# Kernel tuning notes

Hardware: AMD Instinct MI355X
Metric: run time of the kernel (lower is better)

Reference implementation:

```python
import jax, jax.numpy as jnp
import numpy as np

N_NODES = 100000
N_EDGES = 1600000
IN_FEATS = 256
N_HEADS = 4
OUT_FEATS = 32
NEG_SLOPE = 0.2


def setup_inputs() -> dict:
    key = jax.random.key(0)
    k0, k1, k2, k3, k4, k5 = jax.random.split(key, 6)
    feat = jax.random.normal(k0, (N_NODES, IN_FEATS), dtype=jnp.float32)
    src = jax.random.randint(k1, (N_EDGES,), 0, N_NODES, dtype=jnp.int32)
    dst = jax.random.randint(k2, (N_EDGES,), 0, N_NODES, dtype=jnp.int32)
    # fc.weight: [num_heads*out_feats, in_feats] (torch Linear layout)
    W = jax.random.normal(k3, (N_HEADS * OUT_FEATS, IN_FEATS), dtype=jnp.float32) * 0.05
    attn_l = jax.random.normal(k4, (1, N_HEADS, OUT_FEATS), dtype=jnp.float32) * 0.1
    attn_r = jax.random.normal(k5, (1, N_HEADS, OUT_FEATS), dtype=jnp.float32) * 0.1
    return {"feat": feat, "src": src, "dst": dst, "W": W, "attn_l": attn_l, "attn_r": attn_r}


def reference(feat, src, dst, W, attn_l, attn_r):
    N = feat.shape[0]
    H, D = attn_l.shape[1], attn_l.shape[2]
    # fc projection -> [N, H, D]
    feat_src = (feat @ W.T).reshape(N, H, D)
    el = jnp.sum(feat_src * attn_l, axis=-1)  # [N, H]
    er = jnp.sum(feat_src * attn_r, axis=-1)  # [N, H]
    # per-edge scores: u_add_v then LeakyReLU  -> [E, H]
    e = jax.nn.leaky_relu(el[src] + er[dst], negative_slope=NEG_SLOPE)
    # edge_softmax: segmented softmax over edges grouped by destination node
    emax = jax.ops.segment_max(e, dst, num_segments=N)  # [N, H]
    emax = jnp.where(jnp.isfinite(emax), emax, jnp.zeros_like(emax))
    ee = jnp.exp(e - emax[dst])  # [E, H]
    denom = jax.ops.segment_sum(ee, dst, num_segments=N)  # [N, H]
    a = ee / denom[dst]  # [E, H]
    # u_mul_e + sum aggregation -> [N, H, D]
    m = feat_src[src] * a[:, :, None]  # [E, H, D]
    rst = jax.ops.segment_sum(m, dst, num_segments=N)
    return rst
```

## Files before the change

kernel.cpp:

```cpp
#include <hip/hip_runtime.h>
#include <hip/hip_bf16.h>
#include <math.h>

#define NN 100000
#define NE 1600000
#define INF_ 256
#define NH 4
#define DH 32
#define NHD 128
#define NEG_SLOPE 0.2f

#define NBC 391
#define STRIDEC 4608
#define EPBC 8192
#define NBLK_BIN 196
#define GEMM_BLKS 782
#define FMAX 1408
#define SMEM_BYTES 32768

typedef __attribute__((ext_vector_type(8))) short bf16x8;
typedef __attribute__((ext_vector_type(4))) float f32x4;

__device__ __forceinline__ unsigned short f2bf(float f) {
    __hip_bfloat16 b = __float2bfloat16(f);
    return *reinterpret_cast<unsigned short*>(&b);
}

__global__ __launch_bounds__(256) void k_prep0(const float* __restrict__ W,
                                               unsigned short* __restrict__ Wimg,
                                               int* __restrict__ gcurP) {
    int t = threadIdx.x;
    int b = blockIdx.x;
    if (b == 16) {
        for (int i = t; i < NBC; i += 256) gcurP[i * 16] = 0;
        return;
    }
    int i = b * 256 + t;
    int kt = i >> 9;
    int r = (i >> 2) & 127;
    int g = i & 3;
    int slot = g ^ (r & 7);
    const float* s = &W[(size_t)r * INF_ + kt * 32 + g * 8];
    unsigned short tmp[8];
#pragma unroll
    for (int j = 0; j < 8; j++) tmp[j] = f2bf(s[j]);
    *(bf16x8*)&Wimg[(size_t)kt * 8192 + r * 64 + slot * 8] = *(const bf16x8*)tmp;
}

__global__ __launch_bounds__(256) void k_gemmbin(const float* __restrict__ feat,
                                                 const unsigned short* __restrict__ Wimg,
                                                 const int* __restrict__ src,
                                                 const int* __restrict__ dst,
                                                 const float* __restrict__ al,
                                                 const float* __restrict__ ar,
                                                 unsigned short* __restrict__ fsb,
                                                 float* __restrict__ el,
                                                 float* __restrict__ er,
                                                 int* __restrict__ gcurP,
                                                 unsigned* __restrict__ packed) {
    __shared__ __align__(16) char smem[SMEM_BYTES];
    const int t = threadIdx.x;

    if (blockIdx.x >= GEMM_BLKS) {
        int hb = blockIdx.x - GEMM_BLKS;
        int* lc = (int*)smem;
        int* wb = ((int*)smem) + NBC;
        for (int i = t; i < NBC; i += 256) lc[i] = 0;
        __syncthreads();
        int base = hb * EPBC;
#pragma unroll 4
        for (int j = 0; j < 32; j++) {
            int e = base + j * 256 + t;
            if (e < NE) atomicAdd(&lc[dst[e] >> 8], 1);
        }
        __syncthreads();
        for (int i = t; i < NBC; i += 256) {
            int c = lc[i];
            wb[i] = c ? i * STRIDEC + atomicAdd(&gcurP[i * 16], c) : 0;
            lc[i] = 0;
        }
        __syncthreads();
#pragma unroll 4
        for (int j = 0; j < 32; j++) {
            int e = base + j * 256 + t;
            if (e < NE) {
                int d = dst[e];
                int bk = d >> 8;
                int pos = wb[bk] + atomicAdd(&lc[bk], 1);
                if (pos < (bk + 1) * STRIDEC)
                    packed[pos] = ((unsigned)src[e] << 8) | (unsigned)(d & 255);
            }
        }
        return;
    }

    short* sA = (short*)smem;
    short* sB = (short*)(smem + 16384);
    const int brow = blockIdx.x * 128;
    const int wid = t >> 6, lane = t & 63;
    const int wr = wid >> 1, wc = wid & 1;
    const int lg = lane >> 4;
    const int lr = lane & 15;

    f32x4 acc[4][4];
#pragma unroll
    for (int m = 0; m < 4; m++)
#pragma unroll
        for (int n = 0; n < 4; n++) acc[m][n] = (f32x4){0.f, 0.f, 0.f, 0.f};

    const int srow = t >> 1;
    const int cb = (t & 1) * 16;
    const int g0 = cb >> 3;
    const int p0 = (g0 ^ (srow & 7));
    const int p1 = ((g0 + 1) ^ (srow & 7));
    const int grow = brow + srow;
    const bool arow_ok = (grow < NN);
    const char* bimg = (const char*)Wimg;

    float fv[16];
    uint4 wv0, wv1, wv2, wv3;
    if (arow_ok) {
        const float4* pa = (const float4*)&feat[(size_t)grow * INF_ + cb];
        *(float4*)&fv[0] = pa[0];
        *(float4*)&fv[4] = pa[1];
        *(float4*)&fv[8] = pa[2];
        *(float4*)&fv[12] = pa[3];
    } else {
#pragma unroll
        for (int j = 0; j < 16; j++) fv[j] = 0.f;
    }
    wv0 = *(const uint4*)(bimg + t * 16);
    wv1 = *(const uint4*)(bimg + 4096 + t * 16);
    wv2 = *(const uint4*)(bimg + 8192 + t * 16);
    wv3 = *(const uint4*)(bimg + 12288 + t * 16);

    for (int kt = 0; kt < 8; kt++) {
        {
            short sv[16];
#pragma unroll
            for (int j = 0; j < 16; j++) sv[j] = (short)f2bf(fv[j]);
            *(bf16x8*)&sA[srow * 64 + p0 * 8] = *(const bf16x8*)&sv[0];
            *(bf16x8*)&sA[srow * 64 + p1 * 8] = *(const bf16x8*)&sv[8];
            char* bd = (char*)sB;
            *(uint4*)(bd + t * 16) = wv0;
            *(uint4*)(bd + 4096 + t * 16) = wv1;
            *(uint4*)(bd + 8192 + t * 16) = wv2;
            *(uint4*)(bd + 12288 + t * 16) = wv3;
        }
        __syncthreads();
        if (kt < 7) {
            int k0 = (kt + 1) * 32;
            if (arow_ok) {
                const float4* pa = (const float4*)&feat[(size_t)grow * INF_ + k0 + cb];
                *(float4*)&fv[0] = pa[0];
                *(float4*)&fv[4] = pa[1];
                *(float4*)&fv[8] = pa[2];
                *(float4*)&fv[12] = pa[3];
            }
            const char* bsrc = bimg + (size_t)(kt + 1) * 16384;
            wv0 = *(const uint4*)(bsrc + t * 16);
            wv1 = *(const uint4*)(bsrc + 4096 + t * 16);
            wv2 = *(const uint4*)(bsrc + 8192 + t * 16);
            wv3 = *(const uint4*)(bsrc + 12288 + t * 16);
        }
        bf16x8 aF[4], bF[4];
#pragma unroll
        for (int m = 0; m < 4; m++) {
            int r = wr * 64 + m * 16 + lr;
            aF[m] = *(const bf16x8*)&sA[r * 64 + ((lg ^ (r & 7)) * 8)];
        }
#pragma unroll
        for (int n = 0; n < 4; n++) {
            int r = wc * 64 + n * 16 + lr;
            bF[n] = *(const bf16x8*)&sB[r * 64 + ((lg ^ (r & 7)) * 8)];
        }
#pragma unroll
        for (int m = 0; m < 4; m++)
#pragma unroll
            for (int n = 0; n < 4; n++)
                acc[m][n] = __builtin_amdgcn_mfma_f32_16x16x32_bf16(aF[m], bF[n], acc[m][n], 0, 0, 0);
        __syncthreads();
    }
#pragma unroll
    for (int m = 0; m < 4; m++) {
#pragma unroll
        for (int n = 0; n < 4; n++) {
#pragma unroll
            for (int r = 0; r < 4; r++) {
                int gr = brow + wr * 64 + m * 16 + lg * 4 + r;
                if (gr < NN)
                    fsb[(size_t)gr * NHD + wc * 64 + n * 16 + lr] = f2bf(acc[m][n][r]);
            }
        }
    }
    const int hA = wc * 2, hB = wc * 2 + 1;
    const float alA0 = al[hA * 32 + lr], alA1 = al[hA * 32 + 16 + lr];
    const float alB0 = al[hB * 32 + lr], alB1 = al[hB * 32 + 16 + lr];
    const float arA0 = ar[hA * 32 + lr], arA1 = ar[hA * 32 + 16 + lr];
    const float arB0 = ar[hB * 32 + lr], arB1 = ar[hB * 32 + 16 + lr];
#pragma unroll
    for (int m = 0; m < 4; m++) {
#pragma unroll
        for (int r = 0; r < 4; r++) {
            float eA = acc[m][0][r] * alA0 + acc[m][1][r] * alA1;
            float eB = acc[m][2][r] * alB0 + acc[m][3][r] * alB1;
            float fA = acc[m][0][r] * arA0 + acc[m][1][r] * arA1;
            float fB = acc[m][2][r] * arB0 + acc[m][3][r] * arB1;
#pragma unroll
            for (int off = 1; off < 16; off <<= 1) {
                eA += __shfl_xor(eA, off);
                eB += __shfl_xor(eB, off);
                fA += __shfl_xor(fA, off);
                fB += __shfl_xor(fB, off);
            }
            if (lr == 0) {
                int gr = brow + wr * 64 + m * 16 + lg * 4 + r;
                if (gr < NN) {
                    el[gr * 4 + hA] = eA;
                    el[gr * 4 + hB] = eB;
                    er[gr * 4 + hA] = fA;
                    er[gr * 4 + hB] = fB;
                }
            }
        }
    }
}

__global__ __launch_bounds__(256) void k_sortagg(const int* __restrict__ gcurP,
                                                 const unsigned* __restrict__ packed,
                                                 const float* __restrict__ el,
                                                 const float* __restrict__ er,
                                                 const uint4* __restrict__ fsb128,
                                                 float* __restrict__ out) {
    __shared__ int lh[64];
    __shared__ int off[65];
    __shared__ int cur[64];
    __shared__ int esrc_l[FMAX];
    int bq = blockIdx.x;
    int b = bq >> 2, quarter = bq & 3;
    int t = threadIdx.x;
    int beg = b * STRIDEC;
    int cnt = gcurP[b * 16];
    if (cnt > STRIDEC) cnt = STRIDEC;

    if (t < 64) lh[t] = 0;
    __syncthreads();
    for (int k = t; k < cnt; k += 256) {
        unsigned p = packed[beg + k];
        if (((p >> 6) & 3u) == (unsigned)quarter) atomicAdd(&lh[p & 63u], 1);
    }
    __syncthreads();
    if (t < 64) {
        int v = lh[t];
        int x = v;
#pragma unroll
        for (int o = 1; o < 64; o <<= 1) {
            int y = __shfl_up(x, o);
            if (t >= o) x += y;
        }
        off[t] = x - v;
        cur[t] = x - v;
        if (t == 63) off[64] = x;
    }
    __syncthreads();
    for (int k = t; k < cnt; k += 256) {
        unsigned p = packed[beg + k];
        if (((p >> 6) & 3u) == (unsigned)quarter) {
            int pos = atomicAdd(&cur[p & 63u], 1);
            if (pos < FMAX) esrc_l[pos] = (int)(p >> 8);
        }
    }
    __syncthreads();

    int lane = t & 63;
    int wv = t >> 6;
    int q = lane >> 4;
    int sl = lane & 15;
    int h = sl >> 2;

#define STEP(eV, vV)                                           \
    {                                                          \
        float sc_ = (eV) + rr;                                 \
        sc_ = sc_ > 0.f ? sc_ : NEG_SLOPE * sc_;               \
        float ee = __expf(sc_);                                \
        den += ee;                                             \
        a0 += ee * __uint_as_float((vV).x << 16);              \
        a1 += ee * __uint_as_float((vV).x & 0xFFFF0000u);      \
        a2 += ee * __uint_as_float((vV).y << 16);              \
        a3 += ee * __uint_as_float((vV).y & 0xFFFF0000u);      \
        a4 += ee * __uint_as_float((vV).z << 16);              \
        a5 += ee * __uint_as_float((vV).z & 0xFFFF0000u);      \
        a6 += ee * __uint_as_float((vV).w << 16);              \
        a7 += ee * __uint_as_float((vV).w & 0xFFFF0000u);      \
    }

    for (int ln = wv * 16; ln < wv * 16 + 16; ln++) {
        int node = (b << 8) + (quarter << 6) + ln;
        if (node >= NN) break;
        int bg = off[ln];
        int en = off[ln + 1];
        if (en > FMAX) en = FMAX;
        float rr = er[node * 4 + h];
        float den = 0.f;
        float a0 = 0.f, a1 = 0.f, a2 = 0.f, a3 = 0.f;
        float a4 = 0.f, a5 = 0.f, a6 = 0.f, a7 = 0.f;
        int k = bg + q;
        for (; k + 4 < en; k += 8) {
            int s0 = esrc_l[k];
            int s1 = esrc_l[k + 4];
            uint4 v0 = fsb128[(size_t)s0 * 16 + sl];
            uint4 v1 = fsb128[(size_t)s1 * 16 + sl];
            float e0 = el[s0 * 4 + h];
            float e1 = el[s1 * 4 + h];
            STEP(e0, v0)
            STEP(e1, v1)
        }
        for (; k < en; k += 4) {
            int s = esrc_l[k];
            uint4 vv = fsb128[(size_t)s * 16 + sl];
            float eV = el[s * 4 + h];
            STEP(eV, vv)
        }
#pragma unroll
        for (int o = 16; o <= 32; o <<= 1) {
            a0 += __shfl_xor(a0, o);
            a1 += __shfl_xor(a1, o);
            a2 += __shfl_xor(a2, o);
            a3 += __shfl_xor(a3, o);
            a4 += __shfl_xor(a4, o);
            a5 += __shfl_xor(a5, o);
            a6 += __shfl_xor(a6, o);
            a7 += __shfl_xor(a7, o);
            den += __shfl_xor(den, o);
        }
        if (q == 0) {
            float inv = den > 0.f ? 1.0f / den : 0.f;
            float4 o0, o1;
            o0.x = a0 * inv; o0.y = a1 * inv; o0.z = a2 * inv; o0.w = a3 * inv;
            o1.x = a4 * inv; o1.y = a5 * inv; o1.z = a6 * inv; o1.w = a7 * inv;
            float* p = &out[(size_t)node * NHD + sl * 8];
            *(float4*)p = o0;
            *(float4*)(p + 4) = o1;
        }
    }
#undef STEP
}

extern "C" void kernel_launch(void* const* d_in, const int* in_sizes, int n_in,
                              void* d_out, int out_size, void* d_ws, size_t ws_size,
                              hipStream_t stream) {
    const float* feat = (const float*)d_in[0];
    const int* src = (const int*)d_in[1];
    const int* dst = (const int*)d_in[2];
    const float* W = (const float*)d_in[3];
    const float* al = (const float*)d_in[4];
    const float* ar = (const float*)d_in[5];
    float* out = (float*)d_out;

    char* ws = (char*)d_ws;
    unsigned short* fsb = (unsigned short*)ws;   ws += (size_t)NN * NHD * 2;
    unsigned* packed = (unsigned*)ws;            ws += (size_t)NBC * STRIDEC * 4;
    float* el = (float*)ws;                      ws += (size_t)NN * NH * 4;
    float* er = (float*)ws;                      ws += (size_t)NN * NH * 4;
    int* gcurP = (int*)ws;                       ws += (size_t)NBC * 16 * 4;
    unsigned short* Wimg = (unsigned short*)ws;  ws += (size_t)8 * 8192 * 2;

    k_prep0<<<17, 256, 0, stream>>>(W, Wimg, gcurP);
    k_gemmbin<<<GEMM_BLKS + NBLK_BIN, 256, 0, stream>>>(feat, Wimg, src, dst,
                                                        al, ar, fsb, el, er,
                                                        gcurP, packed);
    k_sortagg<<<NBC * 4, 256, 0, stream>>>(gcurP, packed, el, er,
                                           (const uint4*)fsb, out);
}
```

Measured before the change: 151.5 us.

## Stage binned edge records in LDS and scatter them as coalesced runs

```diff
diff --git a/kernel.cpp b/kernel.cpp
--- a/kernel.cpp
+++ b/kernel.cpp
@@ -12,11 +12,11 @@
 
 #define NBC 391
 #define STRIDEC 4608
-#define EPBC 8192
-#define NBLK_BIN 196
+#define EPBC 4096
+#define NBLK_BIN 391
 #define GEMM_BLKS 782
 #define FMAX 1408
-#define SMEM_BYTES 32768
+#define SMEM_BYTES 37504
 
 typedef __attribute__((ext_vector_type(8))) short bf16x8;
 typedef __attribute__((ext_vector_type(4))) float f32x4;
@@ -28,11 +28,11 @@
 
 __global__ __launch_bounds__(256) void k_prep0(const float* __restrict__ W,
                                                unsigned short* __restrict__ Wimg,
-                                               int* __restrict__ gcurP) {
+                                               int* __restrict__ gcur) {
     int t = threadIdx.x;
     int b = blockIdx.x;
     if (b == 16) {
-        for (int i = t; i < NBC; i += 256) gcurP[i * 16] = 0;
+        for (int i = t; i < NBC; i += 256) gcur[i] = 0;
         return;
     }
     int i = b * 256 + t;
@@ -56,40 +56,71 @@
                                                  unsigned short* __restrict__ fsb,
                                                  float* __restrict__ el,
                                                  float* __restrict__ er,
-                                                 int* __restrict__ gcurP,
+                                                 int* __restrict__ gcur,
                                                  unsigned* __restrict__ packed) {
     __shared__ __align__(16) char smem[SMEM_BYTES];
     const int t = threadIdx.x;
 
     if (blockIdx.x >= GEMM_BLKS) {
         int hb = blockIdx.x - GEMM_BLKS;
-        int* lc = (int*)smem;
-        int* wb = ((int*)smem) + NBC;
+        unsigned* lrec = (unsigned*)smem;
+        int* lgpos = (int*)(smem + 16384);
+        int* lc   = (int*)(smem + 32768);
+        int* wb   = lc + NBC;
+        int* loff = wb + NBC;
+        int* wsum = loff + NBC;
         for (int i = t; i < NBC; i += 256) lc[i] = 0;
         __syncthreads();
         int base = hb * EPBC;
 #pragma unroll 4
-        for (int j = 0; j < 32; j++) {
+        for (int j = 0; j < 16; j++) {
             int e = base + j * 256 + t;
             if (e < NE) atomicAdd(&lc[dst[e] >> 8], 1);
         }
         __syncthreads();
+        int i0 = t * 2;
+        int c0 = (i0 < NBC) ? lc[i0] : 0;
+        int c1 = (i0 + 1 < NBC) ? lc[i0 + 1] : 0;
+        int s2 = c0 + c1;
+        int lane = t & 63, w = t >> 6;
+        int x = s2;
+#pragma unroll
+        for (int o = 1; o < 64; o <<= 1) {
+            int y = __shfl_up(x, o);
+            if (lane >= o) x += y;
+        }
+        if (lane == 63) wsum[w] = x;
+        __syncthreads();
+        int add = 0;
+        for (int j = 0; j < w; j++) add += wsum[j];
+        int ex = add + x - s2;
+        if (i0 < NBC) loff[i0] = ex;
+        if (i0 + 1 < NBC) loff[i0 + 1] = ex + c0;
         for (int i = t; i < NBC; i += 256) {
             int c = lc[i];
-            wb[i] = c ? i * STRIDEC + atomicAdd(&gcurP[i * 16], c) : 0;
-            lc[i] = 0;
-        }
+            wb[i] = c ? i * STRIDEC + atomicAdd(&gcur[i], c) : 0;
+        }
+        __syncthreads();
+        for (int i = t; i < NBC; i += 256) lc[i] = loff[i];
         __syncthreads();
 #pragma unroll 4
-        for (int j = 0; j < 32; j++) {
+        for (int j = 0; j < 16; j++) {
             int e = base + j * 256 + t;
             if (e < NE) {
                 int d = dst[e];
                 int bk = d >> 8;
-                int pos = wb[bk] + atomicAdd(&lc[bk], 1);
-                if (pos < (bk + 1) * STRIDEC)
-                    packed[pos] = ((unsigned)src[e] << 8) | (unsigned)(d & 255);
+                int pos = atomicAdd(&lc[bk], 1);
+                lrec[pos] = ((unsigned)src[e] << 8) | (unsigned)(d & 255);
+                int g = wb[bk] + (pos - loff[bk]);
+                lgpos[pos] = (g < (bk + 1) * STRIDEC) ? g : -1;
             }
+        }
+        __syncthreads();
+        int nedge = NE - base;
+        if (nedge > EPBC) nedge = EPBC;
+        for (int i = t; i < nedge; i += 256) {
+            int g = lgpos[i];
+            if (g >= 0) packed[g] = lrec[i];
         }
         return;
     }
@@ -226,7 +257,7 @@
     }
 }
 
-__global__ __launch_bounds__(256) void k_sortagg(const int* __restrict__ gcurP,
+__global__ __launch_bounds__(256) void k_sortagg(const int* __restrict__ gcur,
                                                  const unsigned* __restrict__ packed,
                                                  const float* __restrict__ el,
                                                  const float* __restrict__ er,
@@ -240,7 +271,7 @@
     int b = bq >> 2, quarter = bq & 3;
     int t = threadIdx.x;
     int beg = b * STRIDEC;
-    int cnt = gcurP[b * 16];
+    int cnt = gcur[b];
     if (cnt > STRIDEC) cnt = STRIDEC;
 
     if (t < 64) lh[t] = 0;
@@ -362,13 +393,13 @@
     unsigned* packed = (unsigned*)ws;            ws += (size_t)NBC * STRIDEC * 4;
     float* el = (float*)ws;                      ws += (size_t)NN * NH * 4;
     float* er = (float*)ws;                      ws += (size_t)NN * NH * 4;
-    int* gcurP = (int*)ws;                       ws += (size_t)NBC * 16 * 4;
+    int* gcur = (int*)ws;                        ws += (size_t)NBC * 4;
     unsigned short* Wimg = (unsigned short*)ws;  ws += (size_t)8 * 8192 * 2;
 
-    k_prep0<<<17, 256, 0, stream>>>(W, Wimg, gcurP);
+    k_prep0<<<17, 256, 0, stream>>>(W, Wimg, gcur);
     k_gemmbin<<<GEMM_BLKS + NBLK_BIN, 256, 0, stream>>>(feat, Wimg, src, dst,
                                                         al, ar, fsb, el, er,
-                                                        gcurP, packed);
-    k_sortagg<<<NBC * 4, 256, 0, stream>>>(gcurP, packed, el, er,
+                                                        gcur, packed);
+    k_sortagg<<<NBC * 4, 256, 0, stream>>>(gcur, packed, el, er,
                                            (const uint4*)fsb, out);
 }
```

New measurement: 146.2 us. -3.5%, faster.
